# Optimization experiments

Measured on AMD Instinct MI355X. Metric: run time of the kernel, lower is better.

Reference implementation:

```python
import jax, jax.numpy as jnp
import numpy as np

B, N, DK, DV = 16, 4096, 64, 64


def setup_inputs() -> dict:
    key = jax.random.key(0)
    kq, kk, kv = jax.random.split(key, 3)
    q = jax.random.normal(kq, (B, N, DK), dtype=jnp.float32)
    k = jax.random.normal(kk, (B, N, DK), dtype=jnp.float32)
    v = jax.random.normal(kv, (B, N, DV), dtype=jnp.float32)
    # causal mask: positions j<=i are attendable (mask==True)
    mask = jnp.tril(jnp.ones((N, N), dtype=bool))[None, :, :]  # (1, N, N)
    return {"q": q, "k": k, "v": v, "mask": mask}


def reference(q, k, v, mask):
    # scores: (B, N, N)
    scale = 1.0 / jnp.sqrt(jnp.asarray(q.shape[-1], dtype=q.dtype))
    scores = jnp.einsum('bnd,bmd->bnm', q, k) * scale
    scores = jnp.where(mask, scores, jnp.asarray(-jnp.inf, dtype=scores.dtype))
    attn = jax.nn.softmax(scores, axis=-1)
    # dropout is identity in eval/reference mode
    return jnp.einsum('bnm,bmd->bnd', attn, v)
```

## Files before the change

kernel.cpp:

```cpp
#include <hip/hip_runtime.h>


#define N_SEQ 4096
#define DIM   64

typedef __bf16  bf16x8 __attribute__((ext_vector_type(8)));
typedef unsigned short u16x8 __attribute__((ext_vector_type(8)));
typedef float   f32x4  __attribute__((ext_vector_type(4)));
typedef float   f32x16 __attribute__((ext_vector_type(16)));

static __device__ __forceinline__ unsigned short f2bf(float f) {
    unsigned int u = __float_as_uint(f);
    u += 0x7FFFu + ((u >> 16) & 1u);
    return (unsigned short)(u >> 16);
}

static __device__ __forceinline__ unsigned int pk2bf(float a, float b) {
#if defined(__HIP_DEVICE_COMPILE__) && __has_builtin(__builtin_amdgcn_cvt_pk_bf16_f32)
    typedef __bf16 bf16x2_t __attribute__((ext_vector_type(2)));
    bf16x2_t r = __builtin_amdgcn_cvt_pk_bf16_f32(a, b);
    return __builtin_bit_cast(unsigned int, r);
#else
    return (unsigned int)f2bf(a) | ((unsigned int)f2bf(b) << 16);
#endif
}

static __device__ __forceinline__ float fexp2(float x) {
#if defined(__HIP_DEVICE_COMPILE__) && __has_builtin(__builtin_amdgcn_exp2f)
    return __builtin_amdgcn_exp2f(x);
#else
    return exp2f(x);
#endif
}

static __device__ __forceinline__ bf16x8 ld_frag(const void* p) {
    u16x8 u = *reinterpret_cast<const u16x8*>(p);
    return __builtin_bit_cast(bf16x8, u);
}

static __device__ __forceinline__ f32x16 mfma32(bf16x8 a, bf16x8 b, f32x16 c) {
#if defined(__HIP_DEVICE_COMPILE__)
#if __has_builtin(__builtin_amdgcn_mfma_f32_32x32x16_bf16)
    return __builtin_amdgcn_mfma_f32_32x32x16_bf16(a, b, c, 0, 0, 0);
#else
    f32x16 d;
    asm volatile("v_mfma_f32_32x32x16_bf16 %0, %1, %2, %3"
                 : "=v"(d) : "v"(a), "v"(b), "v"(c));
    return d;
#endif
#else
    (void)a; (void)b;
    return c;
#endif
}

static __device__ __forceinline__ void gl_lds16(const unsigned short* g, unsigned short* l) {
#if defined(__HIP_DEVICE_COMPILE__)
    __builtin_amdgcn_global_load_lds(
        (const __attribute__((address_space(1))) unsigned int*)(g),
        (__attribute__((address_space(3))) unsigned int*)(l), 16, 0, 0);
#else
    (void)g; (void)l;
#endif
}

__global__ __launch_bounds__(256)
void prep_kv(const float* __restrict__ K, const float* __restrict__ V,
             unsigned short* __restrict__ wsK, unsigned short* __restrict__ wsV) {
    const int b = blockIdx.y, t = blockIdx.x;
    if (blockIdx.z == 0) {
        const float* src = K + ((size_t)b * N_SEQ + t * 64) * DIM;
        unsigned short* dst = wsK + ((size_t)(b * 64 + t)) * 4096;
        #pragma unroll
        for (int ph = 0; ph < 2; ++ph) {
            const int gidx = threadIdx.x + ph * 256;
            const int r = gidx >> 3, g = gidx & 7;
            const float* p = src + r * DIM + g * 8;
            f32x4 f0 = *reinterpret_cast<const f32x4*>(p);
            f32x4 f1 = *reinterpret_cast<const f32x4*>(p + 4);
            uint4 w;
            w.x = pk2bf(f0[0], f0[1]); w.y = pk2bf(f0[2], f0[3]);
            w.z = pk2bf(f1[0], f1[1]); w.w = pk2bf(f1[2], f1[3]);
            const int rp = (r & 51) | ((r & 4) << 1) | ((r & 8) >> 1);
            *reinterpret_cast<uint4*>(&dst[(rp * 8 + (g ^ (rp & 7))) * 8]) = w;
        }
    } else {
        const int dv = threadIdx.x & 63;
        const int g0 = threadIdx.x >> 6;
        const float* src = V + ((size_t)b * N_SEQ + t * 64) * DIM + dv;
        unsigned short* dst = wsV + ((size_t)(b * 64 + t)) * 4096 + dv * 64;
        #pragma unroll
        for (int ph = 0; ph < 2; ++ph) {
            const int c = g0 * 2 + ph;
            float p[8];
            #pragma unroll
            for (int e = 0; e < 8; ++e)
                p[e] = src[(size_t)(c * 8 + e) * DIM];
            uint4 w;
            w.x = pk2bf(p[0], p[1]); w.y = pk2bf(p[2], p[3]);
            w.z = pk2bf(p[4], p[5]); w.w = pk2bf(p[6], p[7]);
            *reinterpret_cast<uint4*>(&dst[(c ^ (dv & 7)) * 8]) = w;
        }
    }
}

__global__ __launch_bounds__(256, 2)
void attn_fwd(const float* __restrict__ Q, const unsigned short* __restrict__ wsK,
              const unsigned short* __restrict__ wsV, float* __restrict__ O,
              float* __restrict__ wsO, float* __restrict__ wsL) {
    __shared__ unsigned short kbuf[2][4096];
    __shared__ unsigned short vbuf[2][4096];

    const int tid  = threadIdx.x;
    const int wave = tid >> 6;
    const int lane = tid & 63;
    const int l31  = lane & 31;
    const int h    = lane >> 5;
    const int l7   = lane & 7;
    const int wq   = wave & 1;
    const int wk   = wave >> 1;

    const int L    = (int)blockIdx.x;
    const int r    = L & 7;
    const int w    = L >> 3;
    const int role = w & 1;
    const int bsel = (w >> 1) & 1;
    const int j    = w >> 2;
    const int b    = r * 2 + bsel;
    const int T    = 63 - j;

    int it_tile[2], it_k0[2], it_k1[2], it_half[2], n_items;
    if (role == 0) {
        it_tile[0] = j;  it_k0[0] = 0; it_k1[0] = j + 1;  it_half[0] = -1;
        it_tile[1] = T;  it_k0[1] = 0; it_k1[1] = 31 - j; it_half[1] = 0;
        n_items = 2;
    } else {
        it_tile[0] = T;  it_k0[0] = 31 - j; it_k1[0] = 64 - j; it_half[0] = 1;
        n_items = 1;
    }

    int kaddr[4];
    #pragma unroll
    for (int s = 0; s < 4; ++s)
        kaddr[s] = (wk * 32 + l31) * 128 + (((s * 2 + h) ^ l7) * 16);
    int vbase[2];
    #pragma unroll
    for (int t = 0; t < 2; ++t)
        vbase[t] = l31 * 128 + (((wk * 4 + t * 2 + h) ^ l7) * 16);

    const int dma_off = wave * 1024 + lane * 8;
    const u16x8 ones_u = {0x3F80, 0x3F80, 0x3F80, 0x3F80,
                          0x3F80, 0x3F80, 0x3F80, 0x3F80};
    const bf16x8 ones8 = __builtin_bit_cast(bf16x8, ones_u);
    const float QS = 0.125f * 1.44269504f;

    const unsigned short* kt_src = wsK + (size_t)b * 64 * 4096;
    const unsigned short* vt_src = wsV + (size_t)b * 64 * 4096;

    for (int it = 0; it < n_items; ++it) {
        const int tt   = it_tile[it];
        const int kt0  = it_k0[it];
        const int kt1  = it_k1[it];
        const int half = it_half[it];
        const int i0   = tt * 64;

        __syncthreads();

        f32x16 o_acc[2] = {};
        f32x16 lones = {};

        if (kt0 < kt1) {
            u16x8 qb[4];
            const float* qptr = Q + ((size_t)b * N_SEQ + i0 + wq * 32 + l31) * DIM;
            #pragma unroll
            for (int s = 0; s < 4; ++s) {
                const float* p = qptr + s * 16 + h * 8;
                f32x4 f0 = *reinterpret_cast<const f32x4*>(p);
                f32x4 f1 = *reinterpret_cast<const f32x4*>(p + 4);
                #pragma unroll
                for (int jj = 0; jj < 4; ++jj) {
                    qb[s][jj]     = f2bf(f0[jj] * QS);
                    qb[s][4 + jj] = f2bf(f1[jj] * QS);
                }
            }

            auto dma = [&](int kt, int bufi) {
                const unsigned short* ks = kt_src + (size_t)kt * 4096 + dma_off;
                const unsigned short* vs = vt_src + (size_t)kt * 4096 + dma_off;
                #pragma unroll
                for (int i = 0; i < 2; ++i) {
                    gl_lds16(ks + i * 512, &kbuf[bufi][wave * 1024 + i * 512]);
                    gl_lds16(vs + i * 512, &vbuf[bufi][wave * 1024 + i * 512]);
                }
            };

            auto compute = [&](int kt, const unsigned short* kb, const unsigned short* vb) {
                f32x16 st = {};
                #pragma unroll
                for (int s = 0; s < 4; ++s) {
                    bf16x8 kf = ld_frag((const char*)kb + kaddr[s]);
                    st = mfma32(kf, __builtin_bit_cast(bf16x8, qb[s]), st);
                }
                float pex[16];
                if (kt == tt) {
                    const int qth = wq * 32 + l31 - 8 * h - wk * 32;
                    #pragma unroll
                    for (int rr = 0; rr < 16; ++rr) {
                        const int K0 = (rr & 7) | ((rr & 8) << 1);
                        pex[rr] = fexp2((K0 > qth) ? -3.0e38f : st[rr]);
                    }
                } else {
                    #pragma unroll
                    for (int rr = 0; rr < 16; ++rr)
                        pex[rr] = fexp2(st[rr]);
                }
                unsigned int u[8];
                #pragma unroll
                for (int g = 0; g < 4; ++g) {
                    u[2 * g]     = pk2bf(pex[4 * g],     pex[4 * g + 1]);
                    u[2 * g + 1] = pk2bf(pex[4 * g + 2], pex[4 * g + 3]);
                }
                #pragma unroll
                for (int t = 0; t < 2; ++t) {
                    uint4 aw = make_uint4(u[4 * t], u[4 * t + 1], u[4 * t + 2], u[4 * t + 3]);
                    bf16x8 pa = __builtin_bit_cast(bf16x8, aw);
                    #pragma unroll
                    for (int dvt = 0; dvt < 2; ++dvt) {
                        bf16x8 bv = ld_frag((const char*)vb + vbase[t] + dvt * 4096);
                        o_acc[dvt] = mfma32(pa, bv, o_acc[dvt]);
                    }
                    lones = mfma32(pa, ones8, lones);
                }
            };

            dma(kt0, 0);
            int kt = kt0, bufi = 0;
            while (true) {
                __builtin_amdgcn_s_barrier();
                __builtin_amdgcn_sched_barrier(0);
                if (kt + 1 < kt1) {
                    dma(kt + 1, bufi ^ 1);
                    asm volatile("s_waitcnt vmcnt(4)" ::: "memory");
                } else {
                    asm volatile("s_waitcnt vmcnt(0)" ::: "memory");
                }
                __builtin_amdgcn_sched_barrier(0);
                __builtin_amdgcn_s_barrier();
                __builtin_amdgcn_sched_barrier(0);
                compute(kt, kbuf[bufi], vbuf[bufi]);
                if (++kt == kt1) break;
                bufi ^= 1;
            }
        }

        __syncthreads();
        float* red  = reinterpret_cast<float*>(&kbuf[0][0]);
        float* lred = reinterpret_cast<float*>(&vbuf[0][0]);
        if (wk == 1) {
            #pragma unroll
            for (int rr = 0; rr < 16; ++rr) {
                const int qrow = (rr & 3) + 8 * (rr >> 2) + 4 * h;
                #pragma unroll
                for (int dvt = 0; dvt < 2; ++dvt)
                    red[wq * 2048 + qrow * 64 + dvt * 32 + l31] = o_acc[dvt][rr];
                if (l31 == 0) lred[wq * 32 + qrow] = lones[rr];
            }
        }
        __syncthreads();
        if (wk == 0) {
            if (half < 0) {
                float* obase = O + ((size_t)b * N_SEQ + i0 + wq * 32) * DIM;
                #pragma unroll
                for (int rr = 0; rr < 16; ++rr) {
                    const int qrow = (rr & 3) + 8 * (rr >> 2) + 4 * h;
                    const float lt = lones[rr] + lred[wq * 32 + qrow];
                    const float inv = 1.0f / lt;
                    #pragma unroll
                    for (int dvt = 0; dvt < 2; ++dvt) {
                        const float val = o_acc[dvt][rr]
                            + red[wq * 2048 + qrow * 64 + dvt * 32 + l31];
                        obase[qrow * DIM + dvt * 32 + l31] = val * inv;
                    }
                }
            } else {
                float* po = wsO + (((size_t)(b * 32 + (tt - 32)) * 2 + half) * 4096);
                float* pl = wsL + (((size_t)(b * 32 + (tt - 32)) * 2 + half) * 64);
                #pragma unroll
                for (int rr = 0; rr < 16; ++rr) {
                    const int qrow = (rr & 3) + 8 * (rr >> 2) + 4 * h;
                    const float lt = lones[rr] + lred[wq * 32 + qrow];
                    #pragma unroll
                    for (int dvt = 0; dvt < 2; ++dvt)
                        po[(wq * 32 + qrow) * 64 + dvt * 32 + l31] = o_acc[dvt][rr]
                            + red[wq * 2048 + qrow * 64 + dvt * 32 + l31];
                    if (l31 == 0) pl[wq * 32 + qrow] = lt;
                }
            }
        }
    }
}

__global__ __launch_bounds__(256)
void norm_out(const float* __restrict__ wsO, const float* __restrict__ wsL,
              float* __restrict__ O) {
    const int t = 32 + blockIdx.x, b = blockIdx.y;
    const int row = threadIdx.x >> 2;
    const int c0  = (threadIdx.x & 3) * 16;
    const size_t base = (size_t)(b * 32 + (t - 32)) * 2;
    const float* p0 = wsO + base * 4096 + row * 64 + c0;
    const float* p1 = p0 + 4096;
    const float* l  = wsL + base * 64;
    const float inv = 1.0f / (l[row] + l[64 + row]);
    float* o = O + ((size_t)b * N_SEQ + t * 64 + row) * 64 + c0;
    #pragma unroll
    for (int i = 0; i < 16; i += 4) {
        f32x4 a = *reinterpret_cast<const f32x4*>(p0 + i);
        f32x4 c = *reinterpret_cast<const f32x4*>(p1 + i);
        f32x4 v = (a + c) * inv;
        *reinterpret_cast<f32x4*>(o + i) = v;
    }
}

extern "C" void kernel_launch(void* const* d_in, const int* in_sizes, int n_in,
                              void* d_out, int out_size, void* d_ws, size_t ws_size,
                              hipStream_t stream) {
    const float* q = (const float*)d_in[0];
    const float* k = (const float*)d_in[1];
    const float* v = (const float*)d_in[2];
    float* out = (float*)d_out;

    unsigned short* wsK = (unsigned short*)d_ws;
    unsigned short* wsV = wsK + (size_t)16 * 64 * 4096;
    float* wsO = (float*)(wsV + (size_t)16 * 64 * 4096);
    float* wsL = wsO + (size_t)16 * 32 * 2 * 4096;

    prep_kv<<<dim3(64, 16, 2), dim3(256), 0, stream>>>(k, v, wsK, wsV);
    attn_fwd<<<dim3(1024), dim3(256), 0, stream>>>(q, wsK, wsV, out, wsO, wsL);
    norm_out<<<dim3(32, 16), dim3(256), 0, stream>>>(wsO, wsL, out);
}
```

Before: 206.0 us.

## Use 128-row query tiles with 8-wave blocks sharing each K/V tile

Each block now has 512 threads in eight waves (four along the query dimension, two along the key dimension) and covers a 128-row query tile, so every K/V tile loaded into LDS is reused by twice as many query rows. The grid is halved, work items are reindexed so long and short causal tiles pair up, and the diagonal mask now uses absolute positions because a query tile spans two key tiles. The split-K workspace and norm_out are resized to the 128-row tiles. This reduces K/V global and LDS traffic per query, at the cost of fewer, larger blocks and coarser load balancing at one block per CU.

```diff
diff --git a/kernel.cpp b/kernel.cpp
--- a/kernel.cpp
+++ b/kernel.cpp
@@ -104,12 +104,12 @@
     }
 }
 
-__global__ __launch_bounds__(256, 2)
+__global__ __launch_bounds__(512, 1)
 void attn_fwd(const float* __restrict__ Q, const unsigned short* __restrict__ wsK,
               const unsigned short* __restrict__ wsV, float* __restrict__ O,
               float* __restrict__ wsO, float* __restrict__ wsL) {
-    __shared__ unsigned short kbuf[2][4096];
-    __shared__ unsigned short vbuf[2][4096];
+    __shared__ unsigned short smem[16384];
+    __shared__ float lredX[128];
 
     const int tid  = threadIdx.x;
     const int wave = tid >> 6;
@@ -117,8 +117,8 @@
     const int l31  = lane & 31;
     const int h    = lane >> 5;
     const int l7   = lane & 7;
-    const int wq   = wave & 1;
-    const int wk   = wave >> 1;
+    const int wq   = wave & 3;
+    const int wk   = wave >> 2;
 
     const int L    = (int)blockIdx.x;
     const int r    = L & 7;
@@ -127,15 +127,15 @@
     const int bsel = (w >> 1) & 1;
     const int j    = w >> 2;
     const int b    = r * 2 + bsel;
-    const int T    = 63 - j;
+    const int Tq   = 31 - j;
 
     int it_tile[2], it_k0[2], it_k1[2], it_half[2], n_items;
     if (role == 0) {
-        it_tile[0] = j;  it_k0[0] = 0; it_k1[0] = j + 1;  it_half[0] = -1;
-        it_tile[1] = T;  it_k0[1] = 0; it_k1[1] = 31 - j; it_half[1] = 0;
+        it_tile[0] = j;   it_k0[0] = 0;          it_k1[0] = 2 * j + 2;  it_half[0] = -1;
+        it_tile[1] = Tq;  it_k0[1] = 0;          it_k1[1] = 31 - 2 * j; it_half[1] = 0;
         n_items = 2;
     } else {
-        it_tile[0] = T;  it_k0[0] = 31 - j; it_k1[0] = 64 - j; it_half[0] = 1;
+        it_tile[0] = Tq;  it_k0[0] = 31 - 2 * j; it_k1[0] = 64 - 2 * j; it_half[0] = 1;
         n_items = 1;
     }
 
@@ -148,7 +148,7 @@
     for (int t = 0; t < 2; ++t)
         vbase[t] = l31 * 128 + (((wk * 4 + t * 2 + h) ^ l7) * 16);
 
-    const int dma_off = wave * 1024 + lane * 8;
+    const int dma_off = wave * 512 + lane * 8;
     const u16x8 ones_u = {0x3F80, 0x3F80, 0x3F80, 0x3F80,
                           0x3F80, 0x3F80, 0x3F80, 0x3F80};
     const bf16x8 ones8 = __builtin_bit_cast(bf16x8, ones_u);
@@ -158,11 +158,12 @@
     const unsigned short* vt_src = wsV + (size_t)b * 64 * 4096;
 
     for (int it = 0; it < n_items; ++it) {
-        const int tt   = it_tile[it];
-        const int kt0  = it_k0[it];
-        const int kt1  = it_k1[it];
-        const int half = it_half[it];
-        const int i0   = tt * 64;
+        const int tt    = it_tile[it];
+        const int kt0   = it_k0[it];
+        const int kt1   = it_k1[it];
+        const int half  = it_half[it];
+        const int i0    = tt * 128;
+        const int tdiag = 2 * tt;
 
         __syncthreads();
 
@@ -185,13 +186,10 @@
             }
 
             auto dma = [&](int kt, int bufi) {
-                const unsigned short* ks = kt_src + (size_t)kt * 4096 + dma_off;
-                const unsigned short* vs = vt_src + (size_t)kt * 4096 + dma_off;
-                #pragma unroll
-                for (int i = 0; i < 2; ++i) {
-                    gl_lds16(ks + i * 512, &kbuf[bufi][wave * 1024 + i * 512]);
-                    gl_lds16(vs + i * 512, &vbuf[bufi][wave * 1024 + i * 512]);
-                }
+                gl_lds16(kt_src + (size_t)kt * 4096 + dma_off,
+                         &smem[bufi * 4096 + dma_off]);
+                gl_lds16(vt_src + (size_t)kt * 4096 + dma_off,
+                         &smem[8192 + bufi * 4096 + dma_off]);
             };
 
             auto compute = [&](int kt, const unsigned short* kb, const unsigned short* vb) {
@@ -202,8 +200,8 @@
                     st = mfma32(kf, __builtin_bit_cast(bf16x8, qb[s]), st);
                 }
                 float pex[16];
-                if (kt == tt) {
-                    const int qth = wq * 32 + l31 - 8 * h - wk * 32;
+                if (kt >= tdiag) {
+                    const int qth = (i0 + wq * 32 + l31) - (kt * 64 + wk * 32 + 8 * h);
                     #pragma unroll
                     for (int rr = 0; rr < 16; ++rr) {
                         const int K0 = (rr & 7) | ((rr & 8) << 1);
@@ -240,22 +238,21 @@
                 __builtin_amdgcn_sched_barrier(0);
                 if (kt + 1 < kt1) {
                     dma(kt + 1, bufi ^ 1);
-                    asm volatile("s_waitcnt vmcnt(4)" ::: "memory");
+                    asm volatile("s_waitcnt vmcnt(2)" ::: "memory");
                 } else {
                     asm volatile("s_waitcnt vmcnt(0)" ::: "memory");
                 }
                 __builtin_amdgcn_sched_barrier(0);
                 __builtin_amdgcn_s_barrier();
                 __builtin_amdgcn_sched_barrier(0);
-                compute(kt, kbuf[bufi], vbuf[bufi]);
+                compute(kt, &smem[bufi * 4096], &smem[8192 + bufi * 4096]);
                 if (++kt == kt1) break;
                 bufi ^= 1;
             }
         }
 
         __syncthreads();
-        float* red  = reinterpret_cast<float*>(&kbuf[0][0]);
-        float* lred = reinterpret_cast<float*>(&vbuf[0][0]);
+        float* red = reinterpret_cast<float*>(&smem[0]);
         if (wk == 1) {
             #pragma unroll
             for (int rr = 0; rr < 16; ++rr) {
@@ -263,7 +260,7 @@
                 #pragma unroll
                 for (int dvt = 0; dvt < 2; ++dvt)
                     red[wq * 2048 + qrow * 64 + dvt * 32 + l31] = o_acc[dvt][rr];
-                if (l31 == 0) lred[wq * 32 + qrow] = lones[rr];
+                if (l31 == 0) lredX[wq * 32 + qrow] = lones[rr];
             }
         }
         __syncthreads();
@@ -273,7 +270,7 @@
                 #pragma unroll
                 for (int rr = 0; rr < 16; ++rr) {
                     const int qrow = (rr & 3) + 8 * (rr >> 2) + 4 * h;
-                    const float lt = lones[rr] + lred[wq * 32 + qrow];
+                    const float lt = lones[rr] + lredX[wq * 32 + qrow];
                     const float inv = 1.0f / lt;
                     #pragma unroll
                     for (int dvt = 0; dvt < 2; ++dvt) {
@@ -283,12 +280,12 @@
                     }
                 }
             } else {
-                float* po = wsO + (((size_t)(b * 32 + (tt - 32)) * 2 + half) * 4096);
-                float* pl = wsL + (((size_t)(b * 32 + (tt - 32)) * 2 + half) * 64);
+                float* po = wsO + (((size_t)(b * 16 + (tt - 16)) * 2 + half) * 8192);
+                float* pl = wsL + (((size_t)(b * 16 + (tt - 16)) * 2 + half) * 128);
                 #pragma unroll
                 for (int rr = 0; rr < 16; ++rr) {
                     const int qrow = (rr & 3) + 8 * (rr >> 2) + 4 * h;
-                    const float lt = lones[rr] + lred[wq * 32 + qrow];
+                    const float lt = lones[rr] + lredX[wq * 32 + qrow];
                     #pragma unroll
                     for (int dvt = 0; dvt < 2; ++dvt)
                         po[(wq * 32 + qrow) * 64 + dvt * 32 + l31] = o_acc[dvt][rr]
@@ -303,17 +300,17 @@
 __global__ __launch_bounds__(256)
 void norm_out(const float* __restrict__ wsO, const float* __restrict__ wsL,
               float* __restrict__ O) {
-    const int t = 32 + blockIdx.x, b = blockIdx.y;
-    const int row = threadIdx.x >> 2;
-    const int c0  = (threadIdx.x & 3) * 16;
-    const size_t base = (size_t)(b * 32 + (t - 32)) * 2;
-    const float* p0 = wsO + base * 4096 + row * 64 + c0;
-    const float* p1 = p0 + 4096;
-    const float* l  = wsL + base * 64;
-    const float inv = 1.0f / (l[row] + l[64 + row]);
-    float* o = O + ((size_t)b * N_SEQ + t * 64 + row) * 64 + c0;
+    const int t = 16 + blockIdx.x, b = blockIdx.y;
+    const int row = threadIdx.x >> 1;
+    const int c0  = (threadIdx.x & 1) * 32;
+    const size_t base = (size_t)(b * 16 + (t - 16)) * 2;
+    const float* p0 = wsO + base * 8192 + row * 64 + c0;
+    const float* p1 = p0 + 8192;
+    const float* l  = wsL + base * 128;
+    const float inv = 1.0f / (l[row] + l[128 + row]);
+    float* o = O + ((size_t)b * N_SEQ + t * 128 + row) * 64 + c0;
     #pragma unroll
-    for (int i = 0; i < 16; i += 4) {
+    for (int i = 0; i < 32; i += 4) {
         f32x4 a = *reinterpret_cast<const f32x4*>(p0 + i);
         f32x4 c = *reinterpret_cast<const f32x4*>(p1 + i);
         f32x4 v = (a + c) * inv;
@@ -332,9 +329,9 @@
     unsigned short* wsK = (unsigned short*)d_ws;
     unsigned short* wsV = wsK + (size_t)16 * 64 * 4096;
     float* wsO = (float*)(wsV + (size_t)16 * 64 * 4096);
-    float* wsL = wsO + (size_t)16 * 32 * 2 * 4096;
+    float* wsL = wsO + (size_t)16 * 16 * 2 * 8192;
 
     prep_kv<<<dim3(64, 16, 2), dim3(256), 0, stream>>>(k, v, wsK, wsV);
-    attn_fwd<<<dim3(1024), dim3(256), 0, stream>>>(q, wsK, wsV, out, wsO, wsL);
-    norm_out<<<dim3(32, 16), dim3(256), 0, stream>>>(wsO, wsL, out);
-}
+    attn_fwd<<<dim3(512), dim3(512), 0, stream>>>(q, wsK, wsV, out, wsO, wsL);
+    norm_out<<<dim3(16, 16), dim3(256), 0, stream>>>(wsO, wsL, out);
+}
```

New measurement: 210.4 us. +2.1%, slower.
